# Kernel tuning notes

Hardware: AMD Instinct MI355X
Metric: run time of the kernel (lower is better)

The kernel has to match this reference:

```python
import jax, jax.numpy as jnp
import numpy as np

B = 16384          # batch_size
NF = 50            # n_fields
K = 16             # embedding_dim
V = 1_000_000      # input_dim (vocab)
H = 400            # fc hidden
NNZ = B * NF


def _xavier(key, shape):
    fan_in, fan_out = shape
    lim = (6.0 / (fan_in + fan_out)) ** 0.5
    return jax.random.uniform(key, shape, minval=-lim, maxval=lim, dtype=jnp.float32)


def setup_inputs() -> dict:
    key = jax.random.key(0)
    ks = jax.random.split(key, 12)
    feats = jax.random.randint(ks[0], (NNZ,), 0, V)
    # n_fields contiguous features per sample (required by view(batch_size,-1))
    index = jnp.repeat(jnp.arange(B), NF)
    values = jax.random.uniform(ks[1], (NNZ,), dtype=jnp.float32)
    bias = jnp.zeros((1, 1), jnp.float32)
    weights = _xavier(ks[2], (V, 1))
    embedding = _xavier(ks[3], (V, K))
    d = NF * K  # 800
    W0 = _xavier(ks[4], (d, H))
    b0 = jax.random.normal(ks[5], (1, 1), jnp.float32)
    W1 = _xavier(ks[6], (H, H))
    b1 = jax.random.normal(ks[7], (1, 1), jnp.float32)
    W2 = _xavier(ks[8], (H, 1))
    b2 = jax.random.normal(ks[9], (1, 1), jnp.float32)
    return dict(index=index, feats=feats, values=values, bias=bias,
                weights=weights, embedding=embedding,
                W0=W0, b0=b0, W1=W1, b1=b1, W2=W2, b2=b2, batch_size=B)


def reference(index, feats, values, bias, weights, embedding,
              W0, b0, W1, b1, W2, b2, batch_size):
    # gather (F.embedding)
    w = weights[feats, 0]              # [nnz]
    emb = embedding[feats]             # [nnz, K]

    # first order: segment-sum of w*v, plus bias ([B] + [1,1] -> [1,B], as in torch)
    first = jax.ops.segment_sum(w * values, index, num_segments=batch_size) + bias

    # second order: FM pooling trick, fused over all K dims in one segment reduce
    ev = emb * values[:, None]                                        # [nnz, K]
    s1 = jax.ops.segment_sum(ev, index, num_segments=batch_size)      # [B, K]
    s2 = jax.ops.segment_sum(ev * ev, index, num_segments=batch_size) # [B, K]
    second = 0.5 * jnp.sum(s1 * s1 - s2, axis=1)                      # [B]

    # higher order MLP (relu on every layer, scalar biases)
    x = emb.reshape(batch_size, -1)    # [B, NF*K]
    x = jax.nn.relu(x @ W0 + b0)
    x = jax.nn.relu(x @ W1 + b1)
    x = jax.nn.relu(x @ W2 + b2)       # [B, 1]
    higher = x.reshape(-1)             # [B]

    return jax.nn.sigmoid(first + second + higher)  # [1, B]
```

## Files before the change

### kernel.cpp

```cpp
#include <hip/hip_runtime.h>
#include <hip/hip_bf16.h>


#define BATCH 16384
#define NFLD  50
#define EK    16
#define DDIM  800
#define DPAD  832
#define HDIM  400
#define HPAD  448
#define NPAD  512

typedef __attribute__((ext_vector_type(8))) __bf16 bf16x8;
typedef __attribute__((ext_vector_type(4))) float  f32x4;

typedef const __attribute__((address_space(1))) unsigned int* gas_u32p;
typedef __attribute__((address_space(3))) unsigned int*       las_u32p;

__device__ __forceinline__ void gld_lds16(const void* g, void* l) {
    __builtin_amdgcn_global_load_lds((gas_u32p)g, (las_u32p)l, 16, 0, 0);
}

__global__ __launch_bounds__(256) void transpose_pad_kernel(
    const float* __restrict__ W0, const float* __restrict__ W1,
    __hip_bfloat16* __restrict__ W0t, __hip_bfloat16* __restrict__ W1t)
{
    const int which = blockIdx.z;
    if (which == 1 && blockIdx.x >= HPAD / 32) return;
    const float* src = which ? W1 : W0;
    __hip_bfloat16* dst = which ? W1t : W0t;
    const int srcK = which ? HDIM : DDIM;
    const int srcN = HDIM;
    const int dstCols = which ? HPAD : DPAD;

    __shared__ float tile[32][33];
    const int tx = threadIdx.x & 31, ty = threadIdx.x >> 5;
    const int k0 = blockIdx.x * 32, n0 = blockIdx.y * 32;
#pragma unroll
    for (int r = 0; r < 4; ++r) {
        int k = k0 + ty + r * 8;
        int n = n0 + tx;
        float v = (k < srcK && n < srcN) ? src[(long)k * srcN + n] : 0.f;
        tile[ty + r * 8][tx] = v;
    }
    __syncthreads();
#pragma unroll
    for (int r = 0; r < 4; ++r) {
        int n = n0 + ty + r * 8;
        int k = k0 + tx;
        dst[(long)n * dstCols + k] = __float2bfloat16(tile[tx][ty + r * 8]);
    }
}

__global__ __launch_bounds__(256) void gather_fm_kernel(
    const int* __restrict__ feats, const float* __restrict__ values,
    const float* __restrict__ biasp, const float* __restrict__ weights,
    const float* __restrict__ embedding,
    float* __restrict__ fs, __hip_bfloat16* __restrict__ x)
{
    const int wave = threadIdx.x >> 6;
    const int lane = threadIdx.x & 63;
    const int s    = blockIdx.x * 4 + wave;
    const int r    = lane >> 2, c = lane & 3;
    const long base = (long)s * NFLD;

    int   f = 0; float v = 0.f, wsum = 0.f;
    if (lane < NFLD) {
        f = feats[base + lane];
        v = values[base + lane];
        wsum = weights[f] * v;
    }

    int   fj[4]; float vj[4];
#pragma unroll
    for (int p = 0; p < 4; ++p) {
        const int j = p * 16 + r;
        if (p < 3 || r < 2) { fj[p] = __shfl(f, j); vj[p] = __shfl(v, j); }
    }
    float4 e[4];
#pragma unroll
    for (int p = 0; p < 4; ++p)
        if (p < 3 || r < 2)
            e[p] = *(const float4*)(embedding + (long)fj[p] * EK + c * 4);

    f32x4 s1 = {0.f, 0.f, 0.f, 0.f}, s2 = {0.f, 0.f, 0.f, 0.f};
#pragma unroll
    for (int p = 0; p < 4; ++p) {
        const int j = p * 16 + r;
        if (p < 3 || r < 2) {
            f32x4 ef = {e[p].x, e[p].y, e[p].z, e[p].w};
            f32x4 ev = ef * vj[p];
            s1 += ev;
            s2 += ev * ev;
            __hip_bfloat16 pk[4] = {
                __float2bfloat16(e[p].x), __float2bfloat16(e[p].y),
                __float2bfloat16(e[p].z), __float2bfloat16(e[p].w)};
            *(uint2*)&x[(long)s * DPAD + j * EK + c * 4] = *(uint2*)pk;
        }
    }
    if (lane < 16) *(unsigned int*)&x[(long)s * DPAD + DDIM + lane * 2] = 0u;

#pragma unroll
    for (int m = 4; m <= 32; m <<= 1) {
        s1.x += __shfl_xor(s1.x, m); s1.y += __shfl_xor(s1.y, m);
        s1.z += __shfl_xor(s1.z, m); s1.w += __shfl_xor(s1.w, m);
        s2.x += __shfl_xor(s2.x, m); s2.y += __shfl_xor(s2.y, m);
        s2.z += __shfl_xor(s2.z, m); s2.w += __shfl_xor(s2.w, m);
    }
    float t = (s1.x * s1.x - s2.x) + (s1.y * s1.y - s2.y)
            + (s1.z * s1.z - s2.z) + (s1.w * s1.w - s2.w);
    t += __shfl_xor(t, 1); t += __shfl_xor(t, 2);
    wsum += __shfl_xor(wsum, 1);  wsum += __shfl_xor(wsum, 2);
    wsum += __shfl_xor(wsum, 4);  wsum += __shfl_xor(wsum, 8);
    wsum += __shfl_xor(wsum, 16); wsum += __shfl_xor(wsum, 32);
    if (lane == 0) fs[s] = wsum + 0.5f * t + biasp[0];
}

#define OSTRIDE 136
template <int KDIM, int MODE, int LDC>
__global__ __launch_bounds__(256) void gemm_relu_kernel(
    const __hip_bfloat16* __restrict__ A,
    const __hip_bfloat16* __restrict__ Bt,
    const float* __restrict__ biasp,
    const float* __restrict__ W2,
    void* __restrict__ C)
{
    constexpr int KT = KDIM / 32;
    __shared__ __align__(16) char lds[128 * OSTRIDE * 2];
    __hip_bfloat16* sA = (__hip_bfloat16*)lds;
    __hip_bfloat16* sB = sA + 2 * 4096;
    __hip_bfloat16* sO = (__hip_bfloat16*)lds;

    const int tid  = threadIdx.x;
    const int wave = tid >> 6, lane = tid & 63;
    const int l16  = lane & 15, quad = lane >> 4;
    const int waveM = wave & 1, waveN = wave >> 1;
    const int m0 = blockIdx.y * 128;
    const int n0 = blockIdx.x * 128;

    f32x4 acc[4][4] = {};

    const long ar0 = (long)(m0 + wave * 16 + (lane >> 2)) * KDIM;
    const long ar1 = ar0 + (long)64 * KDIM;
    const long br0 = (long)(n0 + wave * 16 + (lane >> 2)) * KDIM;
    const long br1 = br0 + (long)64 * KDIM;
    const int  ac  = (lane & 3) * 8;
    __hip_bfloat16* ldsA0 = sA + wave * 512 + lane * 8;
    __hip_bfloat16* ldsA1 = sA + 2048 + wave * 512 + lane * 8;
    __hip_bfloat16* ldsB0 = sB + wave * 512 + lane * 8;
    __hip_bfloat16* ldsB1 = sB + 2048 + wave * 512 + lane * 8;

    for (int kt = 0; kt < KT; kt += 2) {
#pragma unroll
        for (int h = 0; h < 2; ++h) {
            const int k0 = (kt + h) * 32;
            gld_lds16(A  + ar0 + k0 + ac, ldsA0 + h * 4096);
            gld_lds16(A  + ar1 + k0 + ac, ldsA1 + h * 4096);
            gld_lds16(Bt + br0 + k0 + ac, ldsB0 + h * 4096);
            gld_lds16(Bt + br1 + k0 + ac, ldsB1 + h * 4096);
        }
        __syncthreads();
#pragma unroll
        for (int h = 0; h < 2; ++h) {
            bf16x8 af[4], bfr[4];
#pragma unroll
            for (int i = 0; i < 4; ++i)
                af[i] = *(const bf16x8*)&sA[h * 4096 + (waveM * 64 + i * 16 + l16) * 32 + quad * 8];
#pragma unroll
            for (int j = 0; j < 4; ++j)
                bfr[j] = *(const bf16x8*)&sB[h * 4096 + (waveN * 64 + j * 16 + l16) * 32 + quad * 8];
#pragma unroll
            for (int i = 0; i < 4; ++i)
#pragma unroll
                for (int j = 0; j < 4; ++j)
                    acc[i][j] = __builtin_amdgcn_mfma_f32_16x16x32_bf16(
                        af[i], bfr[j], acc[i][j], 0, 0, 0);
        }
        __syncthreads();
    }

    const float bias = biasp[0];
    if constexpr (MODE == 0) {
#pragma unroll
        for (int i = 0; i < 4; ++i) {
            const int rl = waveM * 64 + i * 16 + quad * 4;
#pragma unroll
            for (int j = 0; j < 4; ++j) {
                const int cl = waveN * 64 + j * 16 + l16;
                const int gcol = n0 + cl;
#pragma unroll
                for (int r = 0; r < 4; ++r) {
                    float v = acc[i][j][r] + bias;
                    v = v > 0.f ? v : 0.f;
                    if (gcol >= HDIM) v = 0.f;
                    sO[(rl + r) * OSTRIDE + cl] = __float2bfloat16(v);
                }
            }
        }
        __syncthreads();
        __hip_bfloat16* Cp = (__hip_bfloat16*)C;
#pragma unroll
        for (int q = 0; q < 8; ++q) {
            const int flat = tid + q * 256;
            const int rl = flat >> 4, c16 = flat & 15;
            const int gcol = n0 + c16 * 8;
            if (gcol < LDC)
                *(float4*)&Cp[(long)(m0 + rl) * LDC + gcol] =
                    *(const float4*)&sO[rl * OSTRIDE + c16 * 8];
        }
    } else {
        float w2v[4];
#pragma unroll
        for (int j = 0; j < 4; ++j) {
            int col = n0 + waveN * 64 + j * 16 + l16;
            w2v[j] = (col < HDIM) ? W2[col] : 0.f;
        }
        const int slot = blockIdx.x * 2 + waveN;
#pragma unroll
        for (int i = 0; i < 4; ++i) {
#pragma unroll
            for (int r = 0; r < 4; ++r) {
                float p = 0.f;
#pragma unroll
                for (int j = 0; j < 4; ++j) {
                    float v = acc[i][j][r] + bias;
                    v = v > 0.f ? v : 0.f;
                    p += v * w2v[j];
                }
                p += __shfl_xor(p, 1); p += __shfl_xor(p, 2);
                p += __shfl_xor(p, 4); p += __shfl_xor(p, 8);
                if (l16 == 0) {
                    int row = m0 + waveM * 64 + i * 16 + quad * 4 + r;
                    ((float*)C)[(long)row * 8 + slot] = p;
                }
            }
        }
    }
}

__global__ __launch_bounds__(256) void final_kernel(
    const float* __restrict__ partial, const float* __restrict__ b2p,
    const float* __restrict__ fs, float* __restrict__ out)
{
    const int s = blockIdx.x * 256 + threadIdx.x;
    const float4 p0 = *(const float4*)(partial + (long)s * 8);
    const float4 p1 = *(const float4*)(partial + (long)s * 8 + 4);
    float sum = (p0.x + p0.y) + (p0.z + p0.w) + (p1.x + p1.y) + (p1.z + p1.w);
    float h = sum + b2p[0];
    h = h > 0.f ? h : 0.f;
    float z = fs[s] + h;
    out[s] = 1.f / (1.f + __expf(-z));
}

extern "C" void kernel_launch(void* const* d_in, const int* in_sizes, int n_in,
                              void* d_out, int out_size, void* d_ws, size_t ws_size,
                              hipStream_t stream)
{
    const int*   feats     = (const int*)d_in[1];
    const float* values    = (const float*)d_in[2];
    const float* bias      = (const float*)d_in[3];
    const float* weights   = (const float*)d_in[4];
    const float* embedding = (const float*)d_in[5];
    const float* W0 = (const float*)d_in[6];
    const float* b0 = (const float*)d_in[7];
    const float* W1 = (const float*)d_in[8];
    const float* b1 = (const float*)d_in[9];
    const float* W2 = (const float*)d_in[10];
    const float* b2 = (const float*)d_in[11];

    char* ws = (char*)d_ws;
    size_t off = 0;
    auto alloc = [&](size_t bytes) {
        void* p = ws + off;
        off += (bytes + 255) & ~(size_t)255;
        return p;
    };
    float*          fs   = (float*)alloc((size_t)BATCH * 4);
    __hip_bfloat16* x    = (__hip_bfloat16*)alloc((size_t)BATCH * DPAD * 2);
    __hip_bfloat16* h0   = (__hip_bfloat16*)alloc((size_t)BATCH * HPAD * 2);
    float*          part = (float*)alloc((size_t)BATCH * 8 * 4);
    __hip_bfloat16* W0t  = (__hip_bfloat16*)alloc((size_t)NPAD * DPAD * 2);
    __hip_bfloat16* W1t  = (__hip_bfloat16*)alloc((size_t)NPAD * HPAD * 2);
    (void)ws_size; (void)in_sizes; (void)n_in; (void)out_size;

    transpose_pad_kernel<<<dim3(DPAD / 32, NPAD / 32, 2), 256, 0, stream>>>(
        W0, W1, W0t, W1t);
    gather_fm_kernel<<<dim3(BATCH / 4), 256, 0, stream>>>(
        feats, values, bias, weights, embedding, fs, x);
    gemm_relu_kernel<DPAD, 0, HPAD>
        <<<dim3(NPAD / 128, BATCH / 128), 256, 0, stream>>>(
        x, W0t, b0, nullptr, (void*)h0);
    gemm_relu_kernel<HPAD, 1, 8>
        <<<dim3(NPAD / 128, BATCH / 128), 256, 0, stream>>>(
        h0, W1t, b1, W2, (void*)part);
    final_kernel<<<dim3(BATCH / 256), 256, 0, stream>>>(
        part, b2, fs, (float*)d_out);
}
```

Before: 181.2 us.

## Merge weight transpose into gather kernel, widen GEMM k-stage, two samples per wave

Fuses the weight transpose/pad kernel and the gather+FM kernel into one launch, with the first blocks doing transposes and the rest doing gathers. Each gather wave now handles two samples so more embedding loads are in flight. The GEMM k-loop now stages four 32-wide K slices per barrier instead of two. To make that divide evenly, K padding grows (832→896, 448→512), which adds extra zero MACs and memory traffic in exchange for fewer launches and synchronisations.

```diff
diff --git a/kernel.cpp b/kernel.cpp
--- a/kernel.cpp
+++ b/kernel.cpp
@@ -6,10 +6,15 @@
 #define NFLD  50
 #define EK    16
 #define DDIM  800
-#define DPAD  832
+#define DPAD  896
 #define HDIM  400
-#define HPAD  448
+#define HPAD  512
 #define NPAD  512
+
+#define TB_W0 448
+#define TB_W1 256
+#define TBLK  (TB_W0 + TB_W1)
+#define GBLK  (BATCH / 8)
 
 typedef __attribute__((ext_vector_type(8))) __bf16 bf16x8;
 typedef __attribute__((ext_vector_type(4))) float  f32x4;
@@ -21,99 +26,116 @@
     __builtin_amdgcn_global_load_lds((gas_u32p)g, (las_u32p)l, 16, 0, 0);
 }
 
-__global__ __launch_bounds__(256) void transpose_pad_kernel(
+__global__ __launch_bounds__(256) void prep_kernel(
     const float* __restrict__ W0, const float* __restrict__ W1,
-    __hip_bfloat16* __restrict__ W0t, __hip_bfloat16* __restrict__ W1t)
-{
-    const int which = blockIdx.z;
-    if (which == 1 && blockIdx.x >= HPAD / 32) return;
-    const float* src = which ? W1 : W0;
-    __hip_bfloat16* dst = which ? W1t : W0t;
-    const int srcK = which ? HDIM : DDIM;
-    const int srcN = HDIM;
-    const int dstCols = which ? HPAD : DPAD;
-
-    __shared__ float tile[32][33];
-    const int tx = threadIdx.x & 31, ty = threadIdx.x >> 5;
-    const int k0 = blockIdx.x * 32, n0 = blockIdx.y * 32;
-#pragma unroll
-    for (int r = 0; r < 4; ++r) {
-        int k = k0 + ty + r * 8;
-        int n = n0 + tx;
-        float v = (k < srcK && n < srcN) ? src[(long)k * srcN + n] : 0.f;
-        tile[ty + r * 8][tx] = v;
-    }
-    __syncthreads();
-#pragma unroll
-    for (int r = 0; r < 4; ++r) {
-        int n = n0 + ty + r * 8;
-        int k = k0 + tx;
-        dst[(long)n * dstCols + k] = __float2bfloat16(tile[tx][ty + r * 8]);
-    }
-}
-
-__global__ __launch_bounds__(256) void gather_fm_kernel(
+    __hip_bfloat16* __restrict__ W0t, __hip_bfloat16* __restrict__ W1t,
     const int* __restrict__ feats, const float* __restrict__ values,
     const float* __restrict__ biasp, const float* __restrict__ weights,
     const float* __restrict__ embedding,
     float* __restrict__ fs, __hip_bfloat16* __restrict__ x)
 {
+    const int bid = blockIdx.x;
+    if (bid < TBLK) {
+        const int which = bid >= TB_W0;
+        const int i  = which ? bid - TB_W0 : bid;
+        const int nx = which ? 16 : 28;
+        const int bx = i % nx, by = i / nx;
+        const float* src = which ? W1 : W0;
+        __hip_bfloat16* dst = which ? W1t : W0t;
+        const int srcK = which ? HDIM : DDIM;
+        const int dstCols = which ? HPAD : DPAD;
+
+        __shared__ float tile[32][33];
+        const int tx = threadIdx.x & 31, ty = threadIdx.x >> 5;
+        const int k0 = bx * 32, n0 = by * 32;
+#pragma unroll
+        for (int r = 0; r < 4; ++r) {
+            int k = k0 + ty + r * 8;
+            int n = n0 + tx;
+            float v = (k < srcK && n < HDIM) ? src[(long)k * HDIM + n] : 0.f;
+            tile[ty + r * 8][tx] = v;
+        }
+        __syncthreads();
+#pragma unroll
+        for (int r = 0; r < 4; ++r) {
+            int n = n0 + ty + r * 8;
+            int k = k0 + tx;
+            dst[(long)n * dstCols + k] = __float2bfloat16(tile[tx][ty + r * 8]);
+        }
+        return;
+    }
+
     const int wave = threadIdx.x >> 6;
     const int lane = threadIdx.x & 63;
-    const int s    = blockIdx.x * 4 + wave;
     const int r    = lane >> 2, c = lane & 3;
-    const long base = (long)s * NFLD;
-
-    int   f = 0; float v = 0.f, wsum = 0.f;
-    if (lane < NFLD) {
-        f = feats[base + lane];
-        v = values[base + lane];
-        wsum = weights[f] * v;
-    }
-
-    int   fj[4]; float vj[4];
-#pragma unroll
-    for (int p = 0; p < 4; ++p) {
-        const int j = p * 16 + r;
-        if (p < 3 || r < 2) { fj[p] = __shfl(f, j); vj[p] = __shfl(v, j); }
-    }
-    float4 e[4];
-#pragma unroll
-    for (int p = 0; p < 4; ++p)
-        if (p < 3 || r < 2)
-            e[p] = *(const float4*)(embedding + (long)fj[p] * EK + c * 4);
-
-    f32x4 s1 = {0.f, 0.f, 0.f, 0.f}, s2 = {0.f, 0.f, 0.f, 0.f};
-#pragma unroll
-    for (int p = 0; p < 4; ++p) {
-        const int j = p * 16 + r;
-        if (p < 3 || r < 2) {
-            f32x4 ef = {e[p].x, e[p].y, e[p].z, e[p].w};
-            f32x4 ev = ef * vj[p];
-            s1 += ev;
-            s2 += ev * ev;
-            __hip_bfloat16 pk[4] = {
-                __float2bfloat16(e[p].x), __float2bfloat16(e[p].y),
-                __float2bfloat16(e[p].z), __float2bfloat16(e[p].w)};
-            *(uint2*)&x[(long)s * DPAD + j * EK + c * 4] = *(uint2*)pk;
-        }
-    }
-    if (lane < 16) *(unsigned int*)&x[(long)s * DPAD + DDIM + lane * 2] = 0u;
-
-#pragma unroll
-    for (int m = 4; m <= 32; m <<= 1) {
-        s1.x += __shfl_xor(s1.x, m); s1.y += __shfl_xor(s1.y, m);
-        s1.z += __shfl_xor(s1.z, m); s1.w += __shfl_xor(s1.w, m);
-        s2.x += __shfl_xor(s2.x, m); s2.y += __shfl_xor(s2.y, m);
-        s2.z += __shfl_xor(s2.z, m); s2.w += __shfl_xor(s2.w, m);
-    }
-    float t = (s1.x * s1.x - s2.x) + (s1.y * s1.y - s2.y)
-            + (s1.z * s1.z - s2.z) + (s1.w * s1.w - s2.w);
-    t += __shfl_xor(t, 1); t += __shfl_xor(t, 2);
-    wsum += __shfl_xor(wsum, 1);  wsum += __shfl_xor(wsum, 2);
-    wsum += __shfl_xor(wsum, 4);  wsum += __shfl_xor(wsum, 8);
-    wsum += __shfl_xor(wsum, 16); wsum += __shfl_xor(wsum, 32);
-    if (lane == 0) fs[s] = wsum + 0.5f * t + biasp[0];
+    const int sbase = (bid - TBLK) * 8 + wave * 2;
+
+    int   f[2] = {0, 0}; float v[2] = {0.f, 0.f}; float wsum[2] = {0.f, 0.f};
+#pragma unroll
+    for (int q = 0; q < 2; ++q) {
+        const long base = (long)(sbase + q) * NFLD;
+        if (lane < NFLD) {
+            f[q] = feats[base + lane];
+            v[q] = values[base + lane];
+            wsum[q] = weights[f[q]] * v[q];
+        }
+    }
+
+    int   fj[2][4]; float vj[2][4];
+#pragma unroll
+    for (int q = 0; q < 2; ++q)
+#pragma unroll
+        for (int p = 0; p < 4; ++p) {
+            const int j = p * 16 + r;
+            if (p < 3 || r < 2) {
+                fj[q][p] = __shfl(f[q], j);
+                vj[q][p] = __shfl(v[q], j);
+            }
+        }
+    float4 e[2][4];
+#pragma unroll
+    for (int q = 0; q < 2; ++q)
+#pragma unroll
+        for (int p = 0; p < 4; ++p)
+            if (p < 3 || r < 2)
+                e[q][p] = *(const float4*)(embedding + (long)fj[q][p] * EK + c * 4);
+
+#pragma unroll
+    for (int q = 0; q < 2; ++q) {
+        const int s = sbase + q;
+        f32x4 s1 = {0.f, 0.f, 0.f, 0.f}, s2 = {0.f, 0.f, 0.f, 0.f};
+#pragma unroll
+        for (int p = 0; p < 4; ++p) {
+            const int j = p * 16 + r;
+            if (p < 3 || r < 2) {
+                f32x4 ef = {e[q][p].x, e[q][p].y, e[q][p].z, e[q][p].w};
+                f32x4 ev = ef * vj[q][p];
+                s1 += ev;
+                s2 += ev * ev;
+                __hip_bfloat16 pk[4] = {
+                    __float2bfloat16(e[q][p].x), __float2bfloat16(e[q][p].y),
+                    __float2bfloat16(e[q][p].z), __float2bfloat16(e[q][p].w)};
+                *(uint2*)&x[(long)s * DPAD + j * EK + c * 4] = *(uint2*)pk;
+            }
+        }
+        if (lane < 48) *(unsigned int*)&x[(long)s * DPAD + DDIM + lane * 2] = 0u;
+
+#pragma unroll
+        for (int m = 4; m <= 32; m <<= 1) {
+            s1.x += __shfl_xor(s1.x, m); s1.y += __shfl_xor(s1.y, m);
+            s1.z += __shfl_xor(s1.z, m); s1.w += __shfl_xor(s1.w, m);
+            s2.x += __shfl_xor(s2.x, m); s2.y += __shfl_xor(s2.y, m);
+            s2.z += __shfl_xor(s2.z, m); s2.w += __shfl_xor(s2.w, m);
+        }
+        float t = (s1.x * s1.x - s2.x) + (s1.y * s1.y - s2.y)
+                + (s1.z * s1.z - s2.z) + (s1.w * s1.w - s2.w);
+        t += __shfl_xor(t, 1); t += __shfl_xor(t, 2);
+        float w = wsum[q];
+        w += __shfl_xor(w, 1);  w += __shfl_xor(w, 2);
+        w += __shfl_xor(w, 4);  w += __shfl_xor(w, 8);
+        w += __shfl_xor(w, 16); w += __shfl_xor(w, 32);
+        if (lane == 0) fs[s] = w + 0.5f * t + biasp[0];
+    }
 }
 
 #define OSTRIDE 136
@@ -126,9 +148,9 @@
     void* __restrict__ C)
 {
     constexpr int KT = KDIM / 32;
-    __shared__ __align__(16) char lds[128 * OSTRIDE * 2];
+    __shared__ __align__(16) char lds[4 * 8192 * 2];
     __hip_bfloat16* sA = (__hip_bfloat16*)lds;
-    __hip_bfloat16* sB = sA + 2 * 4096;
+    __hip_bfloat16* sB = sA + 4 * 4096;
     __hip_bfloat16* sO = (__hip_bfloat16*)lds;
 
     const int tid  = threadIdx.x;
@@ -150,9 +172,9 @@
     __hip_bfloat16* ldsB0 = sB + wave * 512 + lane * 8;
     __hip_bfloat16* ldsB1 = sB + 2048 + wave * 512 + lane * 8;
 
-    for (int kt = 0; kt < KT; kt += 2) {
-#pragma unroll
-        for (int h = 0; h < 2; ++h) {
+    for (int kt = 0; kt < KT; kt += 4) {
+#pragma unroll
+        for (int h = 0; h < 4; ++h) {
             const int k0 = (kt + h) * 32;
             gld_lds16(A  + ar0 + k0 + ac, ldsA0 + h * 4096);
             gld_lds16(A  + ar1 + k0 + ac, ldsA1 + h * 4096);
@@ -161,7 +183,7 @@
         }
         __syncthreads();
 #pragma unroll
-        for (int h = 0; h < 2; ++h) {
+        for (int h = 0; h < 4; ++h) {
             bf16x8 af[4], bfr[4];
 #pragma unroll
             for (int i = 0; i < 4; ++i)
@@ -283,10 +305,8 @@
     __hip_bfloat16* W1t  = (__hip_bfloat16*)alloc((size_t)NPAD * HPAD * 2);
     (void)ws_size; (void)in_sizes; (void)n_in; (void)out_size;
 
-    transpose_pad_kernel<<<dim3(DPAD / 32, NPAD / 32, 2), 256, 0, stream>>>(
-        W0, W1, W0t, W1t);
-    gather_fm_kernel<<<dim3(BATCH / 4), 256, 0, stream>>>(
-        feats, values, bias, weights, embedding, fs, x);
+    prep_kernel<<<dim3(TBLK + GBLK), 256, 0, stream>>>(
+        W0, W1, W0t, W1t, feats, values, bias, weights, embedding, fs, x);
     gemm_relu_kernel<DPAD, 0, HPAD>
         <<<dim3(NPAD / 128, BATCH / 128), 256, 0, stream>>>(
         x, W0t, b0, nullptr, (void*)h0);
```

After: 183.3 us. No clear change (+1.2%).
